# Kernel tuning notes

Hardware: AMD Instinct MI355X
Metric: run time of the kernel (lower is better)

Reference implementation:

```python
import jax, jax.numpy as jnp
import numpy as np

NB_BINS = 10
N = 33554432  # 2**25 elements


def setup_inputs() -> dict:
    key = jax.random.key(0)
    k1, k2 = jax.random.split(key)
    logits = jax.random.normal(k1, (N,), dtype=jnp.float32)
    labels = jax.random.randint(k2, (N,), 0, 2, dtype=jnp.int32)
    return {"logits": logits, "labels": labels}


def reference(logits, labels):
    # confidences in (0,1); bins are (l, u] over linspace(0,1,nb+1),
    # so bin index = ceil(conf * nb) - 1, clipped to [0, nb-1].
    conf = jax.nn.sigmoid(logits)
    idx = jnp.clip(jnp.ceil(conf * NB_BINS).astype(jnp.int32) - 1, 0, NB_BINS - 1)

    counts = jax.ops.segment_sum(jnp.ones_like(conf), idx, num_segments=NB_BINS)
    sum_conf = jax.ops.segment_sum(conf, idx, num_segments=NB_BINS)
    sum_pos = jax.ops.segment_sum(labels.astype(conf.dtype), idx, num_segments=NB_BINS)

    denom = jnp.maximum(counts, 1.0)
    nonempty = counts > 0
    positives_per_bin = jnp.where(nonempty, sum_pos / denom, 0.0)
    confidence_per_bin = jnp.where(nonempty, sum_conf / denom, 0.0)
    return jnp.stack([positives_per_bin, confidence_per_bin])  # [2, nb_bins]
```

## Files before the change

### kernel.cpp

```cpp
#include <hip/hip_runtime.h>

#define NB 10
#define NCOPY 32
#define SLOTS 20
#define PAD 21
#define CONF_SCALE 65536.0f

typedef unsigned int u32;
typedef unsigned long long u64;

__global__ void rd_zero_ws(u32* __restrict__ ws) {
    int t = threadIdx.x;
    if (t < 40) ws[t] = 0u;
}

__device__ __forceinline__ void rd_acc(float x, int lab, u32* __restrict__ h) {
    float e = __expf(-x);
    float conf = __builtin_amdgcn_rcpf(1.0f + e);
    int b = (int)ceilf(conf * 10.0f) - 1;
    b = min(NB - 1, max(0, b));
    u32 packed = 1u | ((u32)lab << 16);
    u32 cfx = (u32)(conf * CONF_SCALE + 0.5f);
    atomicAdd(&h[b], packed);
    atomicAdd(&h[NB + b], cfx);
}

__global__ __launch_bounds__(256) void rd_hist(const float* __restrict__ logits,
                                               const int* __restrict__ labels,
                                               u32* __restrict__ ws,
                                               long long n) {
    __shared__ u32 hist[NCOPY * PAD];
    for (int i = threadIdx.x; i < NCOPY * PAD; i += blockDim.x) hist[i] = 0u;
    __syncthreads();

    u32* h = &hist[(threadIdx.x & 31) * PAD];

    long long tid    = (long long)blockIdx.x * blockDim.x + threadIdx.x;
    long long stride = (long long)gridDim.x * blockDim.x;
    long long n4     = n >> 2;

    const float4* l4 = (const float4*)logits;
    const int4*   b4 = (const int4*)labels;

    for (long long i = tid; i < n4; i += stride) {
        float4 x = l4[i];
        int4   y = b4[i];
        rd_acc(x.x, y.x, h);
        rd_acc(x.y, y.y, h);
        rd_acc(x.z, y.z, h);
        rd_acc(x.w, y.w, h);
    }
    for (long long i = (n4 << 2) + tid; i < n; i += stride) {
        rd_acc(logits[i], labels[i], h);
    }

    __syncthreads();

    int t = threadIdx.x;
    if (t < SLOTS) {
        u32 s = 0;
        #pragma unroll
        for (int c = 0; c < NCOPY; ++c) s += hist[c * PAD + t];
        u64* conf64 = (u64*)ws;
        u32* cnt    = ws + 20;
        u32* pos    = ws + 30;
        if (t < NB) {
            atomicAdd(&cnt[t], s & 0xFFFFu);
            atomicAdd(&pos[t], s >> 16);
        } else {
            atomicAdd(&conf64[t - NB], (u64)s);
        }
    }
}

__global__ void rd_finalize(const u32* __restrict__ ws, float* __restrict__ out) {
    int b = threadIdx.x;
    if (b < NB) {
        const u64* conf64 = (const u64*)ws;
        float cnt = (float)ws[20 + b];
        float sp  = (float)ws[30 + b];
        float sc  = (float)((double)conf64[b] * (1.0 / 65536.0));
        float denom = fmaxf(cnt, 1.0f);
        bool ne = cnt > 0.0f;
        out[b]      = ne ? (sp / denom) : 0.0f;
        out[NB + b] = ne ? (sc / denom) : 0.0f;
    }
}

extern "C" void kernel_launch(void* const* d_in, const int* in_sizes, int n_in,
                              void* d_out, int out_size, void* d_ws, size_t ws_size,
                              hipStream_t stream) {
    const float* logits = (const float*)d_in[0];
    const int*   labels = (const int*)d_in[1];
    float* out = (float*)d_out;
    u32*   ws  = (u32*)d_ws;
    long long n = (long long)in_sizes[0];

    rd_zero_ws<<<1, 64, 0, stream>>>(ws);
    rd_hist<<<2048, 256, 0, stream>>>(logits, labels, ws, n);
    rd_finalize<<<1, 64, 0, stream>>>(ws, out);
}
```

Baseline: 324.0 us.

## Replace shared-memory atomic histogram with per-thread register accumulators and wave reductions

Drops the per-element LDS atomics into replicated shared histograms. Each thread now keeps counts and positives in packed 6-bit fields of 64-bit registers, flushed every 32 elements, plus per-bin fixed-point confidence sums selected with predicates. Partial results are combined with wave shuffle reductions and a small shared-memory step before the global atomics. This removes LDS atomic contention but adds per-element ALU work for the 10-way select and register pressure. The packed 16-bit count and position fields per block could overflow if a block ever sees 65536 or more elements in one bin; the old code had the same layout.

```diff
diff --git a/kernel.cpp b/kernel.cpp
--- a/kernel.cpp
+++ b/kernel.cpp
@@ -1,75 +1,100 @@
 #include <hip/hip_runtime.h>
-
-#define NB 10
-#define NCOPY 32
-#define SLOTS 20
-#define PAD 21
-#define CONF_SCALE 65536.0f
 
 typedef unsigned int u32;
 typedef unsigned long long u64;
+
+#define NB 10
 
 __global__ void rd_zero_ws(u32* __restrict__ ws) {
     int t = threadIdx.x;
     if (t < 40) ws[t] = 0u;
 }
 
-__device__ __forceinline__ void rd_acc(float x, int lab, u32* __restrict__ h) {
+__device__ __forceinline__ void rd_acc(float x, int lab,
+                                       u64& c64, u64& p64, u32* __restrict__ cacc) {
     float e = __expf(-x);
     float conf = __builtin_amdgcn_rcpf(1.0f + e);
     int b = (int)ceilf(conf * 10.0f) - 1;
     b = min(NB - 1, max(0, b));
-    u32 packed = 1u | ((u32)lab << 16);
-    u32 cfx = (u32)(conf * CONF_SCALE + 0.5f);
-    atomicAdd(&h[b], packed);
-    atomicAdd(&h[NB + b], cfx);
+    u32 cfx = (u32)(conf * 65536.0f + 0.5f);
+
+    u32 sh = (u32)(b * 6);
+    c64 += 1ull << sh;
+    p64 += ((u64)(u32)lab) << sh;
+    #pragma unroll
+    for (int k = 0; k < NB; ++k)
+        cacc[k] += (b == k) ? cfx : 0u;
 }
 
 __global__ __launch_bounds__(256) void rd_hist(const float* __restrict__ logits,
                                                const int* __restrict__ labels,
                                                u32* __restrict__ ws,
                                                long long n) {
-    __shared__ u32 hist[NCOPY * PAD];
-    for (int i = threadIdx.x; i < NCOPY * PAD; i += blockDim.x) hist[i] = 0u;
-    __syncthreads();
-
-    u32* h = &hist[(threadIdx.x & 31) * PAD];
+    u32 cnt[NB], pos[NB], cacc[NB];
+    #pragma unroll
+    for (int b = 0; b < NB; ++b) { cnt[b] = 0u; pos[b] = 0u; cacc[b] = 0u; }
 
     long long tid    = (long long)blockIdx.x * blockDim.x + threadIdx.x;
     long long stride = (long long)gridDim.x * blockDim.x;
     long long n4     = n >> 2;
 
     const float4* l4 = (const float4*)logits;
-    const int4*   b4 = (const int4*)labels;
+    const int4*   i4 = (const int4*)labels;
 
-    for (long long i = tid; i < n4; i += stride) {
-        float4 x = l4[i];
-        int4   y = b4[i];
-        rd_acc(x.x, y.x, h);
-        rd_acc(x.y, y.y, h);
-        rd_acc(x.z, y.z, h);
-        rd_acc(x.w, y.w, h);
-    }
-    for (long long i = (n4 << 2) + tid; i < n; i += stride) {
-        rd_acc(logits[i], labels[i], h);
+    long long i = tid;
+    while (i < n4) {
+        u64 c64 = 0, p64 = 0;
+        for (int sub = 0; sub < 8 && i < n4; ++sub, i += stride) {
+            float4 x = l4[i];
+            int4   y = i4[i];
+            rd_acc(x.x, y.x, c64, p64, cacc);
+            rd_acc(x.y, y.y, c64, p64, cacc);
+            rd_acc(x.z, y.z, c64, p64, cacc);
+            rd_acc(x.w, y.w, c64, p64, cacc);
+        }
+        #pragma unroll
+        for (int b = 0; b < NB; ++b) {
+            cnt[b] += (u32)(c64 >> (6 * b)) & 63u;
+            pos[b] += (u32)(p64 >> (6 * b)) & 63u;
+        }
     }
 
+    long long rem = n4 << 2;
+    if (rem + tid < n) {
+        u64 c64 = 0, p64 = 0;
+        rd_acc(logits[rem + tid], labels[rem + tid], c64, p64, cacc);
+        #pragma unroll
+        for (int b = 0; b < NB; ++b) {
+            cnt[b] += (u32)(c64 >> (6 * b)) & 63u;
+            pos[b] += (u32)(p64 >> (6 * b)) & 63u;
+        }
+    }
+
+    __shared__ u32 s_cp[4][NB];
+    __shared__ u32 s_cf[4][NB];
+    int lane = threadIdx.x & 63;
+    int wave = threadIdx.x >> 6;
+    #pragma unroll
+    for (int b = 0; b < NB; ++b) {
+        u32 cp = (cnt[b] & 0xFFFFu) | (pos[b] << 16);
+        u32 cf = cacc[b];
+        #pragma unroll
+        for (int off = 32; off; off >>= 1) {
+            cp += __shfl_down(cp, off, 64);
+            cf += __shfl_down(cf, off, 64);
+        }
+        if (lane == 0) { s_cp[wave][b] = cp; s_cf[wave][b] = cf; }
+    }
     __syncthreads();
 
-    int t = threadIdx.x;
-    if (t < SLOTS) {
-        u32 s = 0;
-        #pragma unroll
-        for (int c = 0; c < NCOPY; ++c) s += hist[c * PAD + t];
+    if (threadIdx.x < NB) {
+        int b = threadIdx.x;
+        u32 cp = s_cp[0][b] + s_cp[1][b] + s_cp[2][b] + s_cp[3][b];
+        u64 cf = (u64)s_cf[0][b] + s_cf[1][b] + s_cf[2][b] + s_cf[3][b];
         u64* conf64 = (u64*)ws;
-        u32* cnt    = ws + 20;
-        u32* pos    = ws + 30;
-        if (t < NB) {
-            atomicAdd(&cnt[t], s & 0xFFFFu);
-            atomicAdd(&pos[t], s >> 16);
-        } else {
-            atomicAdd(&conf64[t - NB], (u64)s);
-        }
+        atomicAdd(&conf64[b], cf);
+        atomicAdd(&ws[20 + b], cp & 0xFFFFu);
+        atomicAdd(&ws[30 + b], cp >> 16);
     }
 }
 
```

After: 328.2 us. About the same (+1.3%).
